# Kernel optimization log

Measured on AMD Instinct MI355X. Metric: run time of the kernel, lower is better.

The kernel has to match this reference:

```python
import jax, jax.numpy as jnp
import numpy as np

H = 16      # num_head
D = 1024    # feat_dim
DK = D // H # per-head dim
B, S = 2, 2048


def setup_inputs() -> dict:
    key = jax.random.key(0)
    ks = jax.random.split(key, 11)
    scale = 1.0 / np.sqrt(D)
    inp = {
        'query': jax.random.normal(ks[0], (B, S, D), jnp.float32),
        'key':   jax.random.normal(ks[1], (B, S, D), jnp.float32),
        'value': jax.random.normal(ks[2], (B, S, D), jnp.float32),
        # causal lower-triangular mask (seq, seq); 0 entries get -1e9
        'mask':  jnp.tril(jnp.ones((S, S), jnp.int32)),
        # torch nn.Linear params: y = x @ W.T + b
        'w_q': jax.random.normal(ks[3], (D, D), jnp.float32) * scale,
        'b_q': jax.random.normal(ks[4], (D,), jnp.float32) * scale,
        'w_k': jax.random.normal(ks[5], (D, D), jnp.float32) * scale,
        'b_k': jax.random.normal(ks[6], (D,), jnp.float32) * scale,
        'w_v': jax.random.normal(ks[7], (D, D), jnp.float32) * scale,
        'b_v': jax.random.normal(ks[8], (D,), jnp.float32) * scale,
        'w_out': jax.random.normal(ks[9], (D, D), jnp.float32) * scale,
        'b_out': jax.random.normal(ks[10], (D,), jnp.float32) * scale,
    }
    return inp


def reference(query, key, value, mask, w_q, b_q, w_k, b_k, w_v, b_v, w_out, b_out):
    b = query.shape[0]
    # projections + split heads -> (b, h, s, d_k)
    def proj(x, w, bias):
        y = x @ w.T + bias
        return y.reshape(b, -1, H, DK).transpose(0, 2, 1, 3)
    q = proj(query, w_q, b_q)
    k = proj(key, w_k, b_k)
    v = proj(value, w_v, b_v)
    # scaled dot-product attention with materialized score matrix
    scores = jnp.einsum('bhqd,bhkd->bhqk', q, k) / np.sqrt(DK).astype(jnp.float32)
    scores = jnp.where(mask == 0, jnp.float32(-1e9), scores)
    attn = jax.nn.softmax(scores, axis=-1)  # dropout is identity in eval mode
    x = jnp.einsum('bhqk,bhkd->bhqd', attn, v)
    x = x.transpose(0, 2, 1, 3).reshape(b, -1, H * DK)
    return x @ w_out.T + b_out
```

## Files before the change

### kernel.cpp

```cpp
#include <hip/hip_runtime.h>

typedef unsigned short u16;
typedef __attribute__((ext_vector_type(8))) short short8;
typedef __attribute__((ext_vector_type(8))) unsigned short u16x8;
typedef __attribute__((ext_vector_type(4))) float floatx4;

#define S2LOG 0.18033688f

__device__ __forceinline__ u16 f2bf(float f) {
    unsigned int u = __float_as_uint(f);
    return (u16)((u + 0x7FFFu + ((u >> 16) & 1u)) >> 16);
}
__device__ __forceinline__ u16 f2bf_hu(float f) {
    return (u16)((__float_as_uint(f) + 0x8000u) >> 16);
}
__device__ __forceinline__ void gl_lds16(const u16* g, u16* l) {
    __builtin_amdgcn_global_load_lds(
        (const __attribute__((address_space(1))) void*)g,
        (__attribute__((address_space(3))) void*)l, 16, 0, 0);
}

__global__ __launch_bounds__(256) void cvt_all(
    const float* __restrict__ q, const float* __restrict__ k, const float* __restrict__ v,
    const float* __restrict__ wq, const float* __restrict__ wk,
    const float* __restrict__ wv, const float* __restrict__ wo,
    u16* __restrict__ ws)
{
    const int b = blockIdx.x, t = threadIdx.x;
    const float* src; u16* dst; long blk;
    if      (b < 2048) { src = q;  dst = ws;            blk = b; }
    else if (b < 4096) { src = k;  dst = ws + 4194304;  blk = b - 2048; }
    else if (b < 6144) { src = v;  dst = ws + 8388608;  blk = b - 4096; }
    else if (b < 6656) { src = wq; dst = ws + 12582912; blk = b - 6144; }
    else if (b < 7168) { src = wk; dst = ws + 13631488; blk = b - 6656; }
    else if (b < 7680) { src = wv; dst = ws + 14680064; blk = b - 7168; }
    else               { src = wo; dst = ws + 15728640; blk = b - 7680; }
    const long i = blk * 2048 + (long)t * 8;
    const float4 a = *(const float4*)(src + i);
    const float4 c = *(const float4*)(src + i + 4);
    u16x8 o;
    o[0] = f2bf(a.x); o[1] = f2bf(a.y); o[2] = f2bf(a.z); o[3] = f2bf(a.w);
    o[4] = f2bf(c.x); o[5] = f2bf(c.y); o[6] = f2bf(c.z); o[7] = f2bf(c.w);
    *(u16x8*)(dst + i) = o;
}

__device__ __forceinline__ void gemm_core64(
    const u16* __restrict__ A, const u16* __restrict__ Bw,
    int m0, int n0, floatx4 (&acc)[2][4])
{
    __shared__ u16 As[128 * 64];
    __shared__ u16 Bs[64 * 64];
    const int t = threadIdx.x, w = t >> 6;
    const int lane = t & 63, col = lane & 15, quad = lane >> 4;
    const int c7 = col & 7;

#pragma unroll
    for (int i = 0; i < 2; ++i)
#pragma unroll
        for (int j = 0; j < 4; ++j) acc[i][j] = (floatx4)0.f;

    for (int k0 = 0; k0 < 1024; k0 += 64) {
#pragma unroll
        for (int jj = 0; jj < 4; ++jj) {
            const int c = jj * 256 + t;
            const int row = c >> 3, kc = (c & 7) ^ (row & 7);
            gl_lds16(A + (size_t)(m0 + row) * 1024 + k0 + kc * 8,
                     As + (jj * 256 + w * 64) * 8);
        }
#pragma unroll
        for (int jj = 0; jj < 2; ++jj) {
            const int c = jj * 256 + t;
            const int row = c >> 3, kc = (c & 7) ^ (row & 7);
            gl_lds16(Bw + (size_t)(n0 + row) * 1024 + k0 + kc * 8,
                     Bs + (jj * 256 + w * 64) * 8);
        }
        __syncthreads();
#pragma unroll
        for (int ks = 0; ks < 2; ++ks) {
            const int swz = (ks * 4 + quad) ^ c7;
            short8 af[2], bf[4];
#pragma unroll
            for (int i = 0; i < 2; ++i)
                af[i] = *(const short8*)&As[((w * 32 + i * 16 + col) * 8 + swz) * 8];
#pragma unroll
            for (int j = 0; j < 4; ++j)
                bf[j] = *(const short8*)&Bs[((j * 16 + col) * 8 + swz) * 8];
#pragma unroll
            for (int i = 0; i < 2; ++i)
#pragma unroll
                for (int j = 0; j < 4; ++j)
                    acc[i][j] = __builtin_amdgcn_mfma_f32_16x16x32_bf16(
                        af[i], bf[j], acc[i][j], 0, 0, 0);
        }
        __syncthreads();
    }
}

__global__ __launch_bounds__(256) void gemm_qkv(
    const u16* __restrict__ xq, const u16* __restrict__ xk, const u16* __restrict__ xv,
    const u16* __restrict__ wqb, const u16* __restrict__ wkb, const u16* __restrict__ wvb,
    const float* __restrict__ bq, const float* __restrict__ bk, const float* __restrict__ bv,
    u16* __restrict__ Qh, u16* __restrict__ Kh, u16* __restrict__ Vt)
{
    const int z = blockIdx.z;
    const u16*   A    = z == 0 ? xq  : z == 1 ? xk  : xv;
    const u16*   Bw   = z == 0 ? wqb : z == 1 ? wkb : wvb;
    const float* bias = z == 0 ? bq  : z == 1 ? bk  : bv;
    u16*         out  = z == 0 ? Qh  : z == 1 ? Kh  : Vt;
    const float  scale = z == 0 ? S2LOG : 1.0f;
    const int m0 = blockIdx.x * 128, n0 = blockIdx.y * 64;

    floatx4 acc[2][4];
    gemm_core64(A, Bw, m0, n0, acc);

    const int t = threadIdx.x, w = t >> 6;
    const int lane = t & 63, col = lane & 15, quad = lane >> 4;
#pragma unroll
    for (int i = 0; i < 2; ++i)
#pragma unroll
        for (int j = 0; j < 4; ++j)
#pragma unroll
            for (int reg = 0; reg < 4; ++reg) {
                const int gm = m0 + w * 32 + i * 16 + quad * 4 + reg;
                const int gn = n0 + j * 16 + col;
                const float val = (acc[i][j][reg] + bias[gn]) * scale;
                const int bb = gm >> 11, ss = gm & 2047, hh = gn >> 6, dd = gn & 63;
                if (z != 2)
                    out[(((size_t)bb * 16 + hh) * 2048 + ss) * 64 + dd] = f2bf(val);
                else
                    out[(((size_t)bb * 16 + hh) * 64 + dd) * 2048 + ss] = f2bf(val);
            }
}

__global__ __launch_bounds__(256) void gemm_out(
    const u16* __restrict__ A, const u16* __restrict__ Bw,
    const float* __restrict__ bias, float* __restrict__ out)
{
    const int m0 = blockIdx.x * 128, n0 = blockIdx.y * 64;
    floatx4 acc[2][4];
    gemm_core64(A, Bw, m0, n0, acc);
    const int t = threadIdx.x, w = t >> 6;
    const int lane = t & 63, col = lane & 15, quad = lane >> 4;
#pragma unroll
    for (int i = 0; i < 2; ++i)
#pragma unroll
        for (int j = 0; j < 4; ++j)
#pragma unroll
            for (int reg = 0; reg < 4; ++reg) {
                const int gm = m0 + w * 32 + i * 16 + quad * 4 + reg;
                const int gn = n0 + j * 16 + col;
                out[(size_t)gm * 1024 + gn] = acc[i][j][reg] + bias[gn];
            }
}

__global__ __launch_bounds__(256) void attn_mfma(
    const u16* __restrict__ Qh, const u16* __restrict__ Kh,
    const u16* __restrict__ Vt, u16* __restrict__ ctx)
{
    __shared__ u16 QPs[128 * 72];
    __shared__ u16 Ks[2][64 * 64];
    __shared__ u16 Vs[2][64 * 64];
    const int t = threadIdx.x, w = t >> 6;
    const int lane = t & 63, col = lane & 15, quad = lane >> 4;
    const int c7 = col & 7;
    const int bh = blockIdx.y;
    const int qt = (bh < 16) ? (15 - (int)blockIdx.x) : (int)blockIdx.x;
    const int q0 = qt * 128;
    const u16* qg = Qh + ((size_t)bh * 2048 + q0) * 64;
    const u16* kg = Kh + (size_t)bh * 2048 * 64;
    const u16* vg = Vt + (size_t)bh * 2048 * 64;

#pragma unroll
    for (int jj = 0; jj < 4; ++jj) {
        const int c = jj * 256 + t;
        const int row = c >> 3, kc = (c & 7) ^ (row & 7);
        gl_lds16(qg + (size_t)row * 64 + kc * 8, QPs + (jj * 256 + w * 64) * 8);
    }
#pragma unroll
    for (int jj = 0; jj < 2; ++jj) {
        const int c = jj * 256 + t;
        const int row = c >> 3, kc = (c & 7) ^ (row & 7);
        gl_lds16(kg + (size_t)row * 64 + kc * 8, Ks[0] + (jj * 256 + w * 64) * 8);
        gl_lds16(vg + (size_t)row * 2048 + kc * 8, Vs[0] + (jj * 256 + w * 64) * 8);
    }
    __syncthreads();

    short8 qf[2][2];
#pragma unroll
    for (int i = 0; i < 2; ++i)
#pragma unroll
        for (int ks = 0; ks < 2; ++ks)
            qf[i][ks] = *(const short8*)
                &QPs[((w * 32 + i * 16 + col) * 8 + ((ks * 4 + quad) ^ c7)) * 8];
    __syncthreads();

    floatx4 oacc[2][4], lacc[2];
#pragma unroll
    for (int i = 0; i < 2; ++i) {
        lacc[i] = (floatx4)0.f;
#pragma unroll
        for (int j = 0; j < 4; ++j) oacc[i][j] = (floatx4)0.f;
    }
    short8 ones;
#pragma unroll
    for (int i = 0; i < 8; ++i) ones[i] = (short)0x3F80;

    const int ktmax = 2 * qt + 1;
    for (int kt = 0; kt <= ktmax; ++kt) {
        const int cur = kt & 1, nxt = cur ^ 1;
        if (kt < ktmax) {
#pragma unroll
            for (int jj = 0; jj < 2; ++jj) {
                const int c = jj * 256 + t;
                const int row = c >> 3, kc = (c & 7) ^ (row & 7);
                gl_lds16(kg + (size_t)((kt + 1) * 64 + row) * 64 + kc * 8,
                         Ks[nxt] + (jj * 256 + w * 64) * 8);
                gl_lds16(vg + (size_t)row * 2048 + (kt + 1) * 64 + kc * 8,
                         Vs[nxt] + (jj * 256 + w * 64) * 8);
            }
        }
        floatx4 sa[2][4];
#pragma unroll
        for (int i = 0; i < 2; ++i)
#pragma unroll
            for (int j = 0; j < 4; ++j) sa[i][j] = (floatx4)0.f;
#pragma unroll
        for (int ks = 0; ks < 2; ++ks) {
            const int swz = (ks * 4 + quad) ^ c7;
            short8 kf[4];
#pragma unroll
            for (int jc = 0; jc < 4; ++jc)
                kf[jc] = *(const short8*)&Ks[cur][((jc * 16 + col) * 8 + swz) * 8];
#pragma unroll
            for (int i = 0; i < 2; ++i)
#pragma unroll
                for (int jc = 0; jc < 4; ++jc)
                    sa[i][jc] = __builtin_amdgcn_mfma_f32_16x16x32_bf16(
                        qf[i][ks], kf[jc], sa[i][jc], 0, 0, 0);
        }
        const bool pm = (kt >= 2 * qt);
#pragma unroll
        for (int i = 0; i < 2; ++i)
#pragma unroll
            for (int reg = 0; reg < 4; ++reg) {
                const int prow = w * 32 + i * 16 + quad * 4 + reg;
                const int qrow = q0 + prow;
#pragma unroll
                for (int jc = 0; jc < 4; ++jc) {
                    float p = __builtin_amdgcn_exp2f(sa[i][jc][reg]);
                    if (pm && (kt * 64 + jc * 16 + col > qrow)) p = 0.f;
                    QPs[prow * 72 + jc * 16 + col] = f2bf_hu(p);
                }
            }
#pragma unroll
        for (int ks = 0; ks < 2; ++ks) {
            const int swz = (ks * 4 + quad) ^ c7;
            short8 pf[2], vf[4];
#pragma unroll
            for (int i = 0; i < 2; ++i)
                pf[i] = *(const short8*)&QPs[(w * 32 + i * 16 + col) * 72 + ks * 32 + quad * 8];
#pragma unroll
            for (int jd = 0; jd < 4; ++jd)
                vf[jd] = *(const short8*)&Vs[cur][((jd * 16 + col) * 8 + swz) * 8];
#pragma unroll
            for (int i = 0; i < 2; ++i) {
                lacc[i] = __builtin_amdgcn_mfma_f32_16x16x32_bf16(pf[i], ones, lacc[i], 0, 0, 0);
#pragma unroll
                for (int jd = 0; jd < 4; ++jd)
                    oacc[i][jd] = __builtin_amdgcn_mfma_f32_16x16x32_bf16(
                        pf[i], vf[jd], oacc[i][jd], 0, 0, 0);
            }
        }
        __syncthreads();
    }

    const int bb = bh >> 4, hh = bh & 15;
#pragma unroll
    for (int i = 0; i < 2; ++i)
#pragma unroll
        for (int reg = 0; reg < 4; ++reg) {
            const float inv = __builtin_amdgcn_rcpf(lacc[i][reg]);
            const int qrow = q0 + w * 32 + i * 16 + quad * 4 + reg;
#pragma unroll
            for (int jd = 0; jd < 4; ++jd)
                ctx[((size_t)bb * 2048 + qrow) * 1024 + hh * 64 + jd * 16 + col] =
                    f2bf(oacc[i][jd][reg] * inv);
        }
}

extern "C" void kernel_launch(void* const* d_in, const int* in_sizes, int n_in,
                              void* d_out, int out_size, void* d_ws, size_t ws_size,
                              hipStream_t stream)
{
    const float* query = (const float*)d_in[0];
    const float* key   = (const float*)d_in[1];
    const float* value = (const float*)d_in[2];
    const float* w_q   = (const float*)d_in[4];
    const float* b_q   = (const float*)d_in[5];
    const float* w_k   = (const float*)d_in[6];
    const float* b_k   = (const float*)d_in[7];
    const float* w_v   = (const float*)d_in[8];
    const float* b_v   = (const float*)d_in[9];
    const float* w_out = (const float*)d_in[10];
    const float* b_out = (const float*)d_in[11];

    u16* W = (u16*)d_ws;
    u16* xq  = W;
    u16* xk  = W + 4194304;
    u16* xv  = W + 8388608;
    u16* wqb = W + 12582912;
    u16* wkb = W + 13631488;
    u16* wvb = W + 14680064;
    u16* wob = W + 15728640;
    u16* Qh  = W + 16777216;
    u16* Kh  = W + 20971520;
    u16* Vtw = W + 25165824;
    u16* ctx = W + 29360128;

    hipLaunchKernelGGL(cvt_all, dim3(8192), dim3(256), 0, stream,
                       query, key, value, w_q, w_k, w_v, w_out, W);

    hipLaunchKernelGGL(gemm_qkv, dim3(32, 16, 3), dim3(256), 0, stream,
                       xq, xk, xv, wqb, wkb, wvb, b_q, b_k, b_v, Qh, Kh, Vtw);

    hipLaunchKernelGGL(attn_mfma, dim3(16, 32), dim3(256), 0, stream, Qh, Kh, Vtw, ctx);

    hipLaunchKernelGGL(gemm_out, dim3(32, 16), dim3(256), 0, stream,
                       ctx, wob, b_out, (float*)d_out);
}
```

Baseline: 240.4 us.

## Restructure attention to per-wave 16-row tiles loading K/V directly from global

The attention kernel now uses 512 threads with each of 8 waves owning 16 query rows. K and V fragments are read straight from global memory into registers instead of being staged through double-buffered LDS. Only a per-wave swizzled P buffer stays in shared memory, which removes all block-level barriers and lets each wave stop at its own causal limit. In exchange, K/V reuse across waves now relies on the caches rather than LDS, so global/L2 traffic rises and memory latency is no longer hidden by prefetch.

Measured after the change: 309.4 us. +28.7%, slower.

```diff
diff --git a/kernel.cpp b/kernel.cpp
--- a/kernel.cpp
+++ b/kernel.cpp
@@ -153,139 +153,99 @@
             }
 }
 
-__global__ __launch_bounds__(256) void attn_mfma(
+__global__ __launch_bounds__(512, 4) void attn_mfma(
     const u16* __restrict__ Qh, const u16* __restrict__ Kh,
     const u16* __restrict__ Vt, u16* __restrict__ ctx)
 {
-    __shared__ u16 QPs[128 * 72];
-    __shared__ u16 Ks[2][64 * 64];
-    __shared__ u16 Vs[2][64 * 64];
-    const int t = threadIdx.x, w = t >> 6;
-    const int lane = t & 63, col = lane & 15, quad = lane >> 4;
-    const int c7 = col & 7;
+    __shared__ u16 Ps[8 * 1024];
+    const int t = threadIdx.x, w = t >> 6;
+    const int lane = t & 63, col = lane & 15, quad = lane >> 4;
     const int bh = blockIdx.y;
     const int qt = (bh < 16) ? (15 - (int)blockIdx.x) : (int)blockIdx.x;
-    const int q0 = qt * 128;
+    const int q0 = qt * 128 + w * 16;
     const u16* qg = Qh + ((size_t)bh * 2048 + q0) * 64;
     const u16* kg = Kh + (size_t)bh * 2048 * 64;
     const u16* vg = Vt + (size_t)bh * 2048 * 64;
-
-#pragma unroll
-    for (int jj = 0; jj < 4; ++jj) {
-        const int c = jj * 256 + t;
-        const int row = c >> 3, kc = (c & 7) ^ (row & 7);
-        gl_lds16(qg + (size_t)row * 64 + kc * 8, QPs + (jj * 256 + w * 64) * 8);
+    u16* pw = Ps + w * 1024;
+
+    short8 qf[2];
+#pragma unroll
+    for (int ks = 0; ks < 2; ++ks)
+        qf[ks] = *(const short8*)(qg + (size_t)col * 64 + ks * 32 + quad * 8);
+
+    floatx4 oacc[4], lacc;
+    lacc = (floatx4)0.f;
+#pragma unroll
+    for (int j = 0; j < 4; ++j) oacc[j] = (floatx4)0.f;
+    short8 ones;
+#pragma unroll
+    for (int i = 0; i < 8; ++i) ones[i] = (short)0x3F80;
+
+    const int ktmax = (q0 + 15) >> 6;
+    for (int kt = 0; kt <= ktmax; ++kt) {
+        const u16* kb = kg + (size_t)kt * 64 * 64;
+        short8 kf[2][4];
+#pragma unroll
+        for (int ks = 0; ks < 2; ++ks)
+#pragma unroll
+            for (int jc = 0; jc < 4; ++jc)
+                kf[ks][jc] = *(const short8*)
+                    (kb + (size_t)(jc * 16 + col) * 64 + ks * 32 + quad * 8);
+
+        floatx4 sa[4];
+#pragma unroll
+        for (int jc = 0; jc < 4; ++jc) sa[jc] = (floatx4)0.f;
+#pragma unroll
+        for (int ks = 0; ks < 2; ++ks)
+#pragma unroll
+            for (int jc = 0; jc < 4; ++jc)
+                sa[jc] = __builtin_amdgcn_mfma_f32_16x16x32_bf16(
+                    qf[ks], kf[ks][jc], sa[jc], 0, 0, 0);
+
+        const bool pm = (kt == ktmax);
+#pragma unroll
+        for (int reg = 0; reg < 4; ++reg) {
+            const int prow = quad * 4 + reg;
+            const int qrow = q0 + prow;
+            u16* pr = pw + prow * 64 + (col & 7);
+#pragma unroll
+            for (int jc = 0; jc < 4; ++jc) {
+                float p = __builtin_amdgcn_exp2f(sa[jc][reg]);
+                if (pm && (kt * 64 + jc * 16 + col > qrow)) p = 0.f;
+                pr[(((2 * jc + (col >> 3)) ^ (prow & 7))) << 3] = f2bf_hu(p);
+            }
+        }
+
+        short8 vf[2][4];
+#pragma unroll
+        for (int ks = 0; ks < 2; ++ks)
+#pragma unroll
+            for (int jd = 0; jd < 4; ++jd)
+                vf[ks][jd] = *(const short8*)
+                    (vg + (size_t)(jd * 16 + col) * 2048 + kt * 64 + ks * 32 + quad * 8);
+
+#pragma unroll
+        for (int ks = 0; ks < 2; ++ks) {
+            const short8 pf = *(const short8*)
+                (pw + col * 64 + (((ks * 4 + quad) ^ (col & 7)) << 3));
+            lacc = __builtin_amdgcn_mfma_f32_16x16x32_bf16(pf, ones, lacc, 0, 0, 0);
+#pragma unroll
+            for (int jd = 0; jd < 4; ++jd)
+                oacc[jd] = __builtin_amdgcn_mfma_f32_16x16x32_bf16(
+                    pf, vf[ks][jd], oacc[jd], 0, 0, 0);
+        }
     }
-#pragma unroll
-    for (int jj = 0; jj < 2; ++jj) {
-        const int c = jj * 256 + t;
-        const int row = c >> 3, kc = (c & 7) ^ (row & 7);
-        gl_lds16(kg + (size_t)row * 64 + kc * 8, Ks[0] + (jj * 256 + w * 64) * 8);
-        gl_lds16(vg + (size_t)row * 2048 + kc * 8, Vs[0] + (jj * 256 + w * 64) * 8);
+
+    const int bb = bh >> 4, hh = bh & 15;
+#pragma unroll
+    for (int reg = 0; reg < 4; ++reg) {
+        const float inv = __builtin_amdgcn_rcpf(lacc[reg]);
+        const int qrow = q0 + quad * 4 + reg;
+#pragma unroll
+        for (int jd = 0; jd < 4; ++jd)
+            ctx[((size_t)bb * 2048 + qrow) * 1024 + hh * 64 + jd * 16 + col] =
+                f2bf(oacc[jd][reg] * inv);
     }
-    __syncthreads();
-
-    short8 qf[2][2];
-#pragma unroll
-    for (int i = 0; i < 2; ++i)
-#pragma unroll
-        for (int ks = 0; ks < 2; ++ks)
-            qf[i][ks] = *(const short8*)
-                &QPs[((w * 32 + i * 16 + col) * 8 + ((ks * 4 + quad) ^ c7)) * 8];
-    __syncthreads();
-
-    floatx4 oacc[2][4], lacc[2];
-#pragma unroll
-    for (int i = 0; i < 2; ++i) {
-        lacc[i] = (floatx4)0.f;
-#pragma unroll
-        for (int j = 0; j < 4; ++j) oacc[i][j] = (floatx4)0.f;
-    }
-    short8 ones;
-#pragma unroll
-    for (int i = 0; i < 8; ++i) ones[i] = (short)0x3F80;
-
-    const int ktmax = 2 * qt + 1;
-    for (int kt = 0; kt <= ktmax; ++kt) {
-        const int cur = kt & 1, nxt = cur ^ 1;
-        if (kt < ktmax) {
-#pragma unroll
-            for (int jj = 0; jj < 2; ++jj) {
-                const int c = jj * 256 + t;
-                const int row = c >> 3, kc = (c & 7) ^ (row & 7);
-                gl_lds16(kg + (size_t)((kt + 1) * 64 + row) * 64 + kc * 8,
-                         Ks[nxt] + (jj * 256 + w * 64) * 8);
-                gl_lds16(vg + (size_t)row * 2048 + (kt + 1) * 64 + kc * 8,
-                         Vs[nxt] + (jj * 256 + w * 64) * 8);
-            }
-        }
-        floatx4 sa[2][4];
-#pragma unroll
-        for (int i = 0; i < 2; ++i)
-#pragma unroll
-            for (int j = 0; j < 4; ++j) sa[i][j] = (floatx4)0.f;
-#pragma unroll
-        for (int ks = 0; ks < 2; ++ks) {
-            const int swz = (ks * 4 + quad) ^ c7;
-            short8 kf[4];
-#pragma unroll
-            for (int jc = 0; jc < 4; ++jc)
-                kf[jc] = *(const short8*)&Ks[cur][((jc * 16 + col) * 8 + swz) * 8];
-#pragma unroll
-            for (int i = 0; i < 2; ++i)
-#pragma unroll
-                for (int jc = 0; jc < 4; ++jc)
-                    sa[i][jc] = __builtin_amdgcn_mfma_f32_16x16x32_bf16(
-                        qf[i][ks], kf[jc], sa[i][jc], 0, 0, 0);
-        }
-        const bool pm = (kt >= 2 * qt);
-#pragma unroll
-        for (int i = 0; i < 2; ++i)
-#pragma unroll
-            for (int reg = 0; reg < 4; ++reg) {
-                const int prow = w * 32 + i * 16 + quad * 4 + reg;
-                const int qrow = q0 + prow;
-#pragma unroll
-                for (int jc = 0; jc < 4; ++jc) {
-                    float p = __builtin_amdgcn_exp2f(sa[i][jc][reg]);
-                    if (pm && (kt * 64 + jc * 16 + col > qrow)) p = 0.f;
-                    QPs[prow * 72 + jc * 16 + col] = f2bf_hu(p);
-                }
-            }
-#pragma unroll
-        for (int ks = 0; ks < 2; ++ks) {
-            const int swz = (ks * 4 + quad) ^ c7;
-            short8 pf[2], vf[4];
-#pragma unroll
-            for (int i = 0; i < 2; ++i)
-                pf[i] = *(const short8*)&QPs[(w * 32 + i * 16 + col) * 72 + ks * 32 + quad * 8];
-#pragma unroll
-            for (int jd = 0; jd < 4; ++jd)
-                vf[jd] = *(const short8*)&Vs[cur][((jd * 16 + col) * 8 + swz) * 8];
-#pragma unroll
-            for (int i = 0; i < 2; ++i) {
-                lacc[i] = __builtin_amdgcn_mfma_f32_16x16x32_bf16(pf[i], ones, lacc[i], 0, 0, 0);
-#pragma unroll
-                for (int jd = 0; jd < 4; ++jd)
-                    oacc[i][jd] = __builtin_amdgcn_mfma_f32_16x16x32_bf16(
-                        pf[i], vf[jd], oacc[i][jd], 0, 0, 0);
-            }
-        }
-        __syncthreads();
-    }
-
-    const int bb = bh >> 4, hh = bh & 15;
-#pragma unroll
-    for (int i = 0; i < 2; ++i)
-#pragma unroll
-        for (int reg = 0; reg < 4; ++reg) {
-            const float inv = __builtin_amdgcn_rcpf(lacc[i][reg]);
-            const int qrow = q0 + w * 32 + i * 16 + quad * 4 + reg;
-#pragma unroll
-            for (int jd = 0; jd < 4; ++jd)
-                ctx[((size_t)bb * 2048 + qrow) * 1024 + hh * 64 + jd * 16 + col] =
-                    f2bf(oacc[i][jd][reg] * inv);
-        }
 }
 
 extern "C" void kernel_launch(void* const* d_in, const int* in_sizes, int n_in,
@@ -323,7 +283,7 @@
     hipLaunchKernelGGL(gemm_qkv, dim3(32, 16, 3), dim3(256), 0, stream,
                        xq, xk, xv, wqb, wkb, wvb, b_q, b_k, b_v, Qh, Kh, Vtw);
 
-    hipLaunchKernelGGL(attn_mfma, dim3(16, 32), dim3(256), 0, stream, Qh, Kh, Vtw, ctx);
+    hipLaunchKernelGGL(attn_mfma, dim3(16, 32), dim3(512), 0, stream, Qh, Kh, Vtw, ctx);
 
     hipLaunchKernelGGL(gemm_out, dim3(32, 16), dim3(256), 0, stream,
                        ctx, wob, b_out, (float*)d_out);
```
